# Optimization experiments

Measured on AMD Instinct MI355X. Metric: run time of the kernel, lower is better.

Reference implementation:

```python
import jax, jax.numpy as jnp
import numpy as np
import math

IMAGE_SIZE = 256
VIEWING_ANGLE = 30.0  # degrees
NEAR = 0.1
FAR = 100.0
CHUNK = 50


def _look_at(vertices):
    # nr.look_at with at=origin, up=+y, eye from viewing_angle (as in __init__)
    eye = jnp.array([0.0, 0.0, -(1.0 / math.tan(math.radians(VIEWING_ANGLE)) + 1.0)],
                    dtype=vertices.dtype)
    at = jnp.zeros(3, dtype=vertices.dtype)
    up = jnp.array([0.0, 1.0, 0.0], dtype=vertices.dtype)
    z = at - eye
    z = z / jnp.linalg.norm(z)
    x = jnp.cross(up, z)
    x = x / jnp.linalg.norm(x)
    y = jnp.cross(z, x)
    y = y / jnp.linalg.norm(y)
    R = jnp.stack([x, y, z])  # [3,3] rows = camera axes
    return (vertices - eye) @ R.T


def _perspective(v):
    # nr.perspective: x,y divided by z*tan(angle); z (camera depth) kept
    width = math.tan(math.radians(VIEWING_ANGLE))
    z = v[..., 2]
    zs = jnp.where(jnp.abs(z) < 1e-5, 1e-5, z)  # avoid div-by-zero for behind-camera verts
    return jnp.stack([v[..., 0] / (zs * width), v[..., 1] / (zs * width), z], axis=-1)


def reference(vertices, faces):
    """Renderer.forward(vertices, faces, mode='depth'):
    fill_back -> look_at -> perspective -> vertices_to_faces -> rasterize_depth.
    Returns depth image [B, H, W] (FAR where no face covers the pixel)."""
    B = vertices.shape[0]
    # fill_back: append faces with reversed vertex order
    faces2 = jnp.concatenate([faces, faces[:, :, ::-1]], axis=1)  # [B, 2F, 3]
    v_scr = _perspective(_look_at(vertices))                      # [B, V, 3]
    # vertices_to_faces gather
    fv = jax.vmap(lambda v, f: v[f])(v_scr, faces2)               # [B, 2F, 3, 3]
    F2 = fv.shape[1]
    nsteps = F2 // CHUNK
    fv = fv.reshape(B, nsteps, CHUNK, 3, 3).transpose(1, 0, 2, 3, 4)  # [S,B,C,3,3]

    is_ = IMAGE_SIZE
    p = (2.0 * jnp.arange(is_, dtype=vertices.dtype) + 1.0 - is_) / is_  # pixel centers in (-1,1)
    py, px = jnp.meshgrid(p, p, indexing='ij')  # [H,W]

    def step(buf, f):  # f: [B,C,3,3]; z-buffer min over this face chunk
        x = f[..., 0][..., None, None]  # [B,C,3,1,1]
        y = f[..., 1][..., None, None]
        z = f[..., 2]                   # [B,C,3] camera-space depth per vertex
        x0, x1, x2 = x[:, :, 0], x[:, :, 1], x[:, :, 2]
        y0, y1, y2 = y[:, :, 0], y[:, :, 1], y[:, :, 2]
        area = (x1 - x0) * (y2 - y0) - (x2 - x0) * (y1 - y0)  # [B,C,1,1] signed 2*area
        area_s = jnp.where(jnp.abs(area) < 1e-8, 1e-8, area)
        # screen-space barycentric weights (edge functions / area)
        w0 = ((x1 - px) * (y2 - py) - (x2 - px) * (y1 - py)) / area_s
        w1 = ((x2 - px) * (y0 - py) - (x0 - px) * (y2 - py)) / area_s
        w2 = 1.0 - w0 - w1
        zc = jnp.maximum(z, 1e-4)  # safe for masked-out faces only
        # perspective-correct depth: z = 1 / (w0/z0 + w1/z1 + w2/z2)
        inv_z = (w0 / zc[:, :, 0, None, None] + w1 / zc[:, :, 1, None, None]
                 + w2 / zc[:, :, 2, None, None])
        zp = 1.0 / jnp.maximum(inv_z, 1e-6)
        front = jnp.all(z > NEAR, axis=-1)[..., None, None]
        inside = (w0 >= 0) & (w1 >= 0) & (w2 >= 0) & (jnp.abs(area) > 1e-8)
        valid = inside & front & (zp > NEAR) & (zp < FAR)
        zp = jnp.where(valid, zp, FAR)
        return jnp.minimum(buf, jnp.min(zp, axis=1)), None

    buf0 = jnp.full((B, is_, is_), FAR, dtype=vertices.dtype)
    depth, _ = jax.lax.scan(step, buf0, fv)
    return depth


def setup_inputs() -> dict:
    key = jax.random.key(0)
    kv, kf = jax.random.split(key)
    B, NV, NF = 1, 2502, 5000
    # mesh roughly within the camera frustum (eye at z~-2.73 looking at origin)
    vertices = 0.35 * jax.random.normal(kv, (B, NV, 3), dtype=jnp.float32)
    faces = jax.random.randint(kf, (B, NF, 3), 0, NV, dtype=jnp.int32)
    return {"vertices": vertices, "faces": faces}
```

## Files before the change

kernel.cpp:

```cpp
#include <hip/hip_runtime.h>
#include <hip/hip_bf16.h>

#define IS 256
#define NEARV 0.1f
#define FARV 100.0f
#define SLICES 32

__global__ void kv_transform(const float* __restrict__ verts, float4* __restrict__ vout,
                             int* __restrict__ cnt, unsigned int* __restrict__ zb, int nv) {
    int i = blockIdx.x * 256 + threadIdx.x;
    if (i == 0) *cnt = 0;
    zb[i] = 0u;
    if (i >= nv) return;
    float vx = verts[i * 3 + 0];
    float vy = verts[i * 3 + 1];
    float vz = verts[i * 3 + 2];
    float z = vz + 2.7320508075688772f;
    float zs = (fabsf(z) < 1e-5f) ? 1e-5f : z;
    float den = zs * 0.57735026918962576f;
    float sx = vx / den;
    float sy = vy / den;
    float zc = fmaxf(z, 1e-4f);
    float izc = 1.0f / zc;
    vout[i] = make_float4(sx, sy, z, izc);
}

__global__ void kf_faces(const int* __restrict__ faces, const float4* __restrict__ v,
                         float* __restrict__ fd, int* __restrict__ cnt, int nf) {
    int f = blockIdx.x * 256 + threadIdx.x;
    if (f >= nf) return;
    int i0 = faces[f * 3 + 0];
    int i1 = faces[f * 3 + 1];
    int i2 = faces[f * 3 + 2];
    float4 a = v[i0];
    float4 b = v[i1];
    float4 c = v[i2];
    bool front = (a.z > NEARV) && (b.z > NEARV) && (c.z > NEARV);
    float area = (b.x - a.x) * (c.y - a.y) - (c.x - a.x) * (b.y - a.y);
    if (!front || !(fabsf(area) > 1e-8f)) return;
    float xmin = fminf(a.x, fminf(b.x, c.x));
    float xmax = fmaxf(a.x, fmaxf(b.x, c.x));
    float ymin = fminf(a.y, fminf(b.y, c.y));
    float ymax = fmaxf(a.y, fmaxf(b.y, c.y));
    const float PMAX = 255.0f / 256.0f;
    if (xmin > PMAX || xmax < -PMAX || ymin > PMAX || ymax < -PMAX) return;
    float ia = 1.0f / area;
    int k = atomicAdd(cnt, 1);
    float4* o = (float4*)(fd + (size_t)k * 16);
    o[0] = make_float4(a.x, a.y, b.x, b.y);
    o[1] = make_float4(c.x, c.y, ia, a.w);
    o[2] = make_float4(b.w, c.w, 0.0f, 0.0f);
    o[3] = make_float4(xmin, ymin, xmax, ymax);
}

__launch_bounds__(256)
__global__ void kr_raster(const float* __restrict__ fd, const int* __restrict__ cnt,
                          unsigned int* __restrict__ zb) {
    __shared__ float sf[256 * 12];
    __shared__ int scount;
    const int tid = threadIdx.x;
    const int tx = tid & 15;
    const int ty = tid >> 4;
    const int j = blockIdx.x * 16 + tx;
    const int i = blockIdx.y * 16 + ty;
    const float px = ((float)(2 * j + 1) - 256.0f) * (1.0f / 256.0f);
    const float py = ((float)(2 * i + 1) - 256.0f) * (1.0f / 256.0f);
    const float px_lo = ((float)(2 * (blockIdx.x * 16) + 1) - 256.0f) * (1.0f / 256.0f);
    const float px_hi = px_lo + 30.0f / 256.0f;
    const float py_lo = ((float)(2 * (blockIdx.y * 16) + 1) - 256.0f) * (1.0f / 256.0f);
    const float py_hi = py_lo + 30.0f / 256.0f;

    const int nf = *cnt;
    const int per = (nf + SLICES - 1) / SLICES;
    const int f0 = blockIdx.z * per;
    const int f1 = min(nf, f0 + per);

    float maxinv = 0.0f;

    for (int base = f0; base < f1; base += 256) {
        if (tid == 0) scount = 0;
        __syncthreads();
        int f = base + tid;
        if (f < f1) {
            const float4* p = (const float4*)(fd + (size_t)f * 16);
            float4 bb = p[3];
            if (bb.x <= px_hi && bb.z >= px_lo && bb.y <= py_hi && bb.w >= py_lo) {
                float4 d0 = p[0];
                float4 d1 = p[1];
                float4 d2 = p[2];
                int k = atomicAdd(&scount, 1);
                float4* q = (float4*)(sf + k * 12);
                q[0] = d0;
                q[1] = d1;
                q[2] = d2;
            }
        }
        __syncthreads();
        const int m = scount;
#pragma unroll 2
        for (int k = 0; k < m; ++k) {
            const float4* q = (const float4*)(sf + k * 12);
            float4 d0 = q[0];
            float4 d1 = q[1];
            float4 d2 = q[2];
            float x0 = d0.x, y0 = d0.y, x1 = d0.z, y1 = d0.w;
            float x2 = d1.x, y2 = d1.y, ia = d1.z;
            float iz0 = d1.w, iz1 = d2.x, iz2 = d2.y;
            float dx0 = x0 - px, dx1 = x1 - px, dx2 = x2 - px;
            float dy0 = y0 - py, dy1 = y1 - py, dy2 = y2 - py;
            float e0 = dx1 * dy2 - dx2 * dy1;
            float e1 = dx2 * dy0 - dx0 * dy2;
            float w0 = e0 * ia;
            float w1 = e1 * ia;
            float w2 = 1.0f - w0 - w1;
            float invz = w0 * iz0 + w1 * iz1 + w2 * iz2;
            float invzc = fmaxf(invz, 1e-6f);
            bool ok = (w0 >= 0.0f) && (w1 >= 0.0f) && (w2 >= 0.0f) &&
                      (invzc < 10.0f) && (invzc > 0.01f);
            if (ok) maxinv = fmaxf(maxinv, invzc);
        }
        __syncthreads();
    }
    if (maxinv > 0.0f) atomicMax(&zb[i * IS + j], __float_as_uint(maxinv));
}

__global__ void kfin(unsigned int* __restrict__ zb, float* __restrict__ out) {
    int p = blockIdx.x * 256 + threadIdx.x;
    unsigned int m = zb[p];
    out[p] = (m != 0u) ? (1.0f / __uint_as_float(m)) : FARV;
}

extern "C" void kernel_launch(void* const* d_in, const int* in_sizes, int n_in,
                              void* d_out, int out_size, void* d_ws, size_t ws_size,
                              hipStream_t stream) {
    const float* verts = (const float*)d_in[0];
    const int* faces = (const int*)d_in[1];
    float* out = (float*)d_out;
    unsigned int* zb = (unsigned int*)d_out;

    const int nv = in_sizes[0] / 3;
    const int nf = in_sizes[1] / 3;

    char* ws = (char*)d_ws;
    int* cnt = (int*)ws;
    float4* vtx = (float4*)(ws + 256);
    size_t fd_off = 256 + (((size_t)nv * 16 + 255) & ~(size_t)255);
    float* fd = (float*)(ws + fd_off);

    kv_transform<<<(IS * IS) / 256, 256, 0, stream>>>(verts, vtx, cnt, zb, nv);
    kf_faces<<<(nf + 255) / 256, 256, 0, stream>>>(faces, vtx, fd, cnt, nf);
    kr_raster<<<dim3(16, 16, SLICES), 256, 0, stream>>>(fd, cnt, zb);
    kfin<<<(IS * IS) / 256, 256, 0, stream>>>(zb, out);
}
```

Baseline: 112.2 us.

## Fuse vertex transform and face setup into persistent atomic-queue rasterizer

Drops the separate vertex-transform, face-setup and finalize kernels. A persistent rasterizer pulls (tile, slice) work items from a global atomic counter, and each block recomputes projected vertices and face setup from raw inputs for its slice. The z-buffer is initialised to FAR and updated with atomicMin on depth, which removes the finalize pass. Launch count and intermediate buffer traffic go down, at the cost of redundant per-tile face setup (every face is transformed 256 times) and of culling only after the gather.

```diff
diff --git a/kernel.cpp b/kernel.cpp
--- a/kernel.cpp
+++ b/kernel.cpp
@@ -5,129 +5,124 @@
 #define NEARV 0.1f
 #define FARV 100.0f
 #define SLICES 32
+#define NTILES 256
+#define NITEMS (NTILES * SLICES)
 
-__global__ void kv_transform(const float* __restrict__ verts, float4* __restrict__ vout,
-                             int* __restrict__ cnt, unsigned int* __restrict__ zb, int nv) {
+__global__ void kinit(unsigned int* __restrict__ zb, int* __restrict__ work) {
     int i = blockIdx.x * 256 + threadIdx.x;
-    if (i == 0) *cnt = 0;
-    zb[i] = 0u;
-    if (i >= nv) return;
-    float vx = verts[i * 3 + 0];
-    float vy = verts[i * 3 + 1];
-    float vz = verts[i * 3 + 2];
-    float z = vz + 2.7320508075688772f;
-    float zs = (fabsf(z) < 1e-5f) ? 1e-5f : z;
-    float den = zs * 0.57735026918962576f;
-    float sx = vx / den;
-    float sy = vy / den;
-    float zc = fmaxf(z, 1e-4f);
-    float izc = 1.0f / zc;
-    vout[i] = make_float4(sx, sy, z, izc);
+    zb[i] = 0x42C80000u;
+    if (i == 0) *work = 0;
 }
 
-__global__ void kf_faces(const int* __restrict__ faces, const float4* __restrict__ v,
-                         float* __restrict__ fd, int* __restrict__ cnt, int nf) {
-    int f = blockIdx.x * 256 + threadIdx.x;
-    if (f >= nf) return;
-    int i0 = faces[f * 3 + 0];
-    int i1 = faces[f * 3 + 1];
-    int i2 = faces[f * 3 + 2];
-    float4 a = v[i0];
-    float4 b = v[i1];
-    float4 c = v[i2];
-    bool front = (a.z > NEARV) && (b.z > NEARV) && (c.z > NEARV);
-    float area = (b.x - a.x) * (c.y - a.y) - (c.x - a.x) * (b.y - a.y);
-    if (!front || !(fabsf(area) > 1e-8f)) return;
-    float xmin = fminf(a.x, fminf(b.x, c.x));
-    float xmax = fmaxf(a.x, fmaxf(b.x, c.x));
-    float ymin = fminf(a.y, fminf(b.y, c.y));
-    float ymax = fmaxf(a.y, fmaxf(b.y, c.y));
-    const float PMAX = 255.0f / 256.0f;
-    if (xmin > PMAX || xmax < -PMAX || ymin > PMAX || ymax < -PMAX) return;
-    float ia = 1.0f / area;
-    int k = atomicAdd(cnt, 1);
-    float4* o = (float4*)(fd + (size_t)k * 16);
-    o[0] = make_float4(a.x, a.y, b.x, b.y);
-    o[1] = make_float4(c.x, c.y, ia, a.w);
-    o[2] = make_float4(b.w, c.w, 0.0f, 0.0f);
-    o[3] = make_float4(xmin, ymin, xmax, ymax);
-}
+__launch_bounds__(256, 8)
+__global__ void kraster(const float* __restrict__ verts, const int* __restrict__ faces,
+                        unsigned int* __restrict__ zb, int* __restrict__ work, int nf) {
+    __shared__ __align__(16) float sf[256 * 12];
+    __shared__ int scount;
+    __shared__ int sitem;
 
-__launch_bounds__(256)
-__global__ void kr_raster(const float* __restrict__ fd, const int* __restrict__ cnt,
-                          unsigned int* __restrict__ zb) {
-    __shared__ float sf[256 * 12];
-    __shared__ int scount;
     const int tid = threadIdx.x;
     const int tx = tid & 15;
     const int ty = tid >> 4;
-    const int j = blockIdx.x * 16 + tx;
-    const int i = blockIdx.y * 16 + ty;
-    const float px = ((float)(2 * j + 1) - 256.0f) * (1.0f / 256.0f);
-    const float py = ((float)(2 * i + 1) - 256.0f) * (1.0f / 256.0f);
-    const float px_lo = ((float)(2 * (blockIdx.x * 16) + 1) - 256.0f) * (1.0f / 256.0f);
-    const float px_hi = px_lo + 30.0f / 256.0f;
-    const float py_lo = ((float)(2 * (blockIdx.y * 16) + 1) - 256.0f) * (1.0f / 256.0f);
-    const float py_hi = py_lo + 30.0f / 256.0f;
+    const int per = (nf + SLICES - 1) / SLICES;
 
-    const int nf = *cnt;
-    const int per = (nf + SLICES - 1) / SLICES;
-    const int f0 = blockIdx.z * per;
-    const int f1 = min(nf, f0 + per);
-
-    float maxinv = 0.0f;
-
-    for (int base = f0; base < f1; base += 256) {
-        if (tid == 0) scount = 0;
-        __syncthreads();
-        int f = base + tid;
-        if (f < f1) {
-            const float4* p = (const float4*)(fd + (size_t)f * 16);
-            float4 bb = p[3];
-            if (bb.x <= px_hi && bb.z >= px_lo && bb.y <= py_hi && bb.w >= py_lo) {
-                float4 d0 = p[0];
-                float4 d1 = p[1];
-                float4 d2 = p[2];
-                int k = atomicAdd(&scount, 1);
-                float4* q = (float4*)(sf + k * 12);
-                q[0] = d0;
-                q[1] = d1;
-                q[2] = d2;
-            }
+    for (;;) {
+        if (tid == 0) {
+            sitem = atomicAdd(work, 1);
+            scount = 0;
         }
         __syncthreads();
-        const int m = scount;
+        const int item = sitem;
+        if (item >= NITEMS) break;
+        const int tile = item & (NTILES - 1);
+        const int slice = item >> 8;
+        const int bx = tile & 15;
+        const int by = tile >> 4;
+        const int j = bx * 16 + tx;
+        const int i = by * 16 + ty;
+        const float px = ((float)(2 * j + 1) - 256.0f) * (1.0f / 256.0f);
+        const float py = ((float)(2 * i + 1) - 256.0f) * (1.0f / 256.0f);
+        const float px_lo = ((float)(2 * (bx * 16) + 1) - 256.0f) * (1.0f / 256.0f);
+        const float px_hi = px_lo + 30.0f / 256.0f;
+        const float py_lo = ((float)(2 * (by * 16) + 1) - 256.0f) * (1.0f / 256.0f);
+        const float py_hi = py_lo + 30.0f / 256.0f;
+
+        const int f0 = slice * per;
+        const int f1 = min(nf, f0 + per);
+
+        float maxinv = 0.0f;
+
+        for (int base = f0; base < f1; base += 256) {
+            int f = base + tid;
+            if (f < f1) {
+                int i0 = faces[f * 3 + 0];
+                int i1 = faces[f * 3 + 1];
+                int i2 = faces[f * 3 + 2];
+                float z0 = verts[i0 * 3 + 2] + 2.7320508075688772f;
+                float z1 = verts[i1 * 3 + 2] + 2.7320508075688772f;
+                float z2 = verts[i2 * 3 + 2] + 2.7320508075688772f;
+                bool front = (z0 > NEARV) && (z1 > NEARV) && (z2 > NEARV);
+                float zs0 = (fabsf(z0) < 1e-5f) ? 1e-5f : z0;
+                float zs1 = (fabsf(z1) < 1e-5f) ? 1e-5f : z1;
+                float zs2 = (fabsf(z2) < 1e-5f) ? 1e-5f : z2;
+                float d0 = zs0 * 0.57735026918962576f;
+                float d1 = zs1 * 0.57735026918962576f;
+                float d2 = zs2 * 0.57735026918962576f;
+                float x0 = verts[i0 * 3 + 0] / d0;
+                float y0 = verts[i0 * 3 + 1] / d0;
+                float x1 = verts[i1 * 3 + 0] / d1;
+                float y1 = verts[i1 * 3 + 1] / d1;
+                float x2 = verts[i2 * 3 + 0] / d2;
+                float y2 = verts[i2 * 3 + 1] / d2;
+                float area = (x1 - x0) * (y2 - y0) - (x2 - x0) * (y1 - y0);
+                if (front && (fabsf(area) > 1e-8f)) {
+                    float xmin = fminf(x0, fminf(x1, x2));
+                    float xmax = fmaxf(x0, fmaxf(x1, x2));
+                    float ymin = fminf(y0, fminf(y1, y2));
+                    float ymax = fmaxf(y0, fmaxf(y1, y2));
+                    if (xmin <= px_hi && xmax >= px_lo && ymin <= py_hi && ymax >= py_lo) {
+                        float ia = 1.0f / area;
+                        float iz0 = 1.0f / fmaxf(z0, 1e-4f);
+                        float iz1 = 1.0f / fmaxf(z1, 1e-4f);
+                        float iz2 = 1.0f / fmaxf(z2, 1e-4f);
+                        int k = atomicAdd(&scount, 1);
+                        float4* q = (float4*)(sf + k * 12);
+                        q[0] = make_float4(x0, y0, x1, y1);
+                        q[1] = make_float4(x2, y2, ia, iz0);
+                        q[2] = make_float4(iz1, iz2, 0.0f, 0.0f);
+                    }
+                }
+            }
+            __syncthreads();
+            const int m = scount;
 #pragma unroll 2
-        for (int k = 0; k < m; ++k) {
-            const float4* q = (const float4*)(sf + k * 12);
-            float4 d0 = q[0];
-            float4 d1 = q[1];
-            float4 d2 = q[2];
-            float x0 = d0.x, y0 = d0.y, x1 = d0.z, y1 = d0.w;
-            float x2 = d1.x, y2 = d1.y, ia = d1.z;
-            float iz0 = d1.w, iz1 = d2.x, iz2 = d2.y;
-            float dx0 = x0 - px, dx1 = x1 - px, dx2 = x2 - px;
-            float dy0 = y0 - py, dy1 = y1 - py, dy2 = y2 - py;
-            float e0 = dx1 * dy2 - dx2 * dy1;
-            float e1 = dx2 * dy0 - dx0 * dy2;
-            float w0 = e0 * ia;
-            float w1 = e1 * ia;
-            float w2 = 1.0f - w0 - w1;
-            float invz = w0 * iz0 + w1 * iz1 + w2 * iz2;
-            float invzc = fmaxf(invz, 1e-6f);
-            bool ok = (w0 >= 0.0f) && (w1 >= 0.0f) && (w2 >= 0.0f) &&
-                      (invzc < 10.0f) && (invzc > 0.01f);
-            if (ok) maxinv = fmaxf(maxinv, invzc);
+            for (int k = 0; k < m; ++k) {
+                const float4* q = (const float4*)(sf + k * 12);
+                float4 a0 = q[0];
+                float4 a1 = q[1];
+                float4 a2 = q[2];
+                float dx0 = a0.x - px, dy0 = a0.y - py;
+                float dx1 = a0.z - px, dy1 = a0.w - py;
+                float dx2 = a1.x - px, dy2 = a1.y - py;
+                float e0 = dx1 * dy2 - dx2 * dy1;
+                float e1 = dx2 * dy0 - dx0 * dy2;
+                float w0 = e0 * a1.z;
+                float w1 = e1 * a1.z;
+                float w2 = 1.0f - w0 - w1;
+                float invz = w0 * a1.w + w1 * a2.x + w2 * a2.y;
+                float invzc = fmaxf(invz, 1e-6f);
+                bool ok = (w0 >= 0.0f) && (w1 >= 0.0f) && (w2 >= 0.0f) &&
+                          (invzc < 10.0f) && (invzc > 0.01f);
+                if (ok) maxinv = fmaxf(maxinv, invzc);
+            }
+            __syncthreads();
+            if (tid == 0) scount = 0;
         }
-        __syncthreads();
+        if (maxinv > 0.0f) {
+            float zp = 1.0f / maxinv;
+            atomicMin(&zb[i * IS + j], __float_as_uint(zp));
+        }
     }
-    if (maxinv > 0.0f) atomicMax(&zb[i * IS + j], __float_as_uint(maxinv));
-}
-
-__global__ void kfin(unsigned int* __restrict__ zb, float* __restrict__ out) {
-    int p = blockIdx.x * 256 + threadIdx.x;
-    unsigned int m = zb[p];
-    out[p] = (m != 0u) ? (1.0f / __uint_as_float(m)) : FARV;
 }
 
 extern "C" void kernel_launch(void* const* d_in, const int* in_sizes, int n_in,
@@ -135,20 +130,12 @@
                               hipStream_t stream) {
     const float* verts = (const float*)d_in[0];
     const int* faces = (const int*)d_in[1];
-    float* out = (float*)d_out;
     unsigned int* zb = (unsigned int*)d_out;
 
-    const int nv = in_sizes[0] / 3;
     const int nf = in_sizes[1] / 3;
 
-    char* ws = (char*)d_ws;
-    int* cnt = (int*)ws;
-    float4* vtx = (float4*)(ws + 256);
-    size_t fd_off = 256 + (((size_t)nv * 16 + 255) & ~(size_t)255);
-    float* fd = (float*)(ws + fd_off);
+    int* work = (int*)d_ws;
 
-    kv_transform<<<(IS * IS) / 256, 256, 0, stream>>>(verts, vtx, cnt, zb, nv);
-    kf_faces<<<(nf + 255) / 256, 256, 0, stream>>>(faces, vtx, fd, cnt, nf);
-    kr_raster<<<dim3(16, 16, SLICES), 256, 0, stream>>>(fd, cnt, zb);
-    kfin<<<(IS * IS) / 256, 256, 0, stream>>>(zb, out);
+    kinit<<<(IS * IS) / 256, 256, 0, stream>>>(zb, work);
+    kraster<<<2048, 256, 0, stream>>>(verts, faces, zb, work, nf);
 }
```

Result: slower. 177.4 us (+58.2%).
